# Performance work log

Measured on AMD Instinct MI355X. Metric: run time of the kernel, lower is better.

## Reference

```python
import jax, jax.numpy as jnp
import numpy as np

NUM_CLASSES = 1000
FEAT = 192
HID = 256
TOTAL_NODES = 8192  # 16 images * 512 patches, kNN is global (no batch vector in source)


def _knn_idx(x, k):
    # squared euclidean distances, top-k smallest (self-loop included: d(i,i)=0)
    sq = jnp.sum(x * x, axis=-1)                       # [N]
    d = sq[:, None] + sq[None, :] - 2.0 * (x @ x.T)    # [N, N]
    _, idx = jax.lax.top_k(-d, k)                      # [N, k] neighbor indices per node
    return idx


def _sage_conv(x, idx, w_l, b_l, w_r):
    # PyG SAGEConv (mean aggr): lin_l(mean_j x_j) + lin_r(x_i); bias on lin_l
    agg = jnp.mean(x[idx], axis=1)                     # [N, C_in] mean over k neighbors
    return agg @ w_l + b_l + x @ w_r


def setup_inputs() -> dict:
    key = jax.random.key(0)
    ks = jax.random.split(key, 8)
    s = lambda fi, fo: (2.0 / (fi + fo)) ** 0.5
    return {
        "x": jax.random.normal(ks[0], (TOTAL_NODES, FEAT), dtype=jnp.float32),
        "w_l0": jax.random.normal(ks[1], (FEAT, HID), jnp.float32) * s(FEAT, HID),
        "b_l0": jnp.zeros((HID,), jnp.float32),
        "w_r0": jax.random.normal(ks[2], (FEAT, HID), jnp.float32) * s(FEAT, HID),
        "w_l1": jax.random.normal(ks[3], (HID, HID), jnp.float32) * s(HID, HID),
        "b_l1": jnp.zeros((HID,), jnp.float32),
        "w_r1": jax.random.normal(ks[4], (HID, HID), jnp.float32) * s(HID, HID),
        "w_l2": jax.random.normal(ks[5], (HID, NUM_CLASSES), jnp.float32) * s(HID, NUM_CLASSES),
        "b_l2": jnp.zeros((NUM_CLASSES,), jnp.float32),
        "w_r2": jax.random.normal(ks[6], (HID, NUM_CLASSES), jnp.float32) * s(HID, NUM_CLASSES),
        "k": 9,
        "batch_size": 16,
    }


def reference(x, w_l0, b_l0, w_r0, w_l1, b_l1, w_r1, w_l2, b_l2, w_r2, k, batch_size):
    idx = _knn_idx(x, k)  # graph built once from input features, reused by all layers
    h = jax.nn.relu(_sage_conv(x, idx, w_l0, b_l0, w_r0))
    h = jax.nn.relu(_sage_conv(h, idx, w_l1, b_l1, w_r1))
    h = jax.nn.relu(_sage_conv(h, idx, w_l2, b_l2, w_r2))
    # global_mean_pool with batch = arange(B).repeat_interleave(N/B): equal-size segments
    h = h.reshape(batch_size, -1, h.shape[-1]).mean(axis=1)  # [B, num_classes]
    return h
```

## Files before the change

kernel.cpp:

```cpp
#include <hip/hip_runtime.h>

#define NN   8192
#define FEAT 192
#define HID  256
#define NCLS 1000
#define KNN  9
#define NPP  512
#define NIMG 16
#define KD   192
#define KL0  384

typedef unsigned short ushort_t;
typedef unsigned int uint_t;
typedef __attribute__((ext_vector_type(8))) __bf16 bf16x8;
typedef __attribute__((ext_vector_type(4))) float f32x4;

#define ASYNC16(gptr, lptr)                                                  \
  __builtin_amdgcn_global_load_lds(                                          \
      (const __attribute__((address_space(1))) void*)(gptr),                 \
      (__attribute__((address_space(3))) void*)(lptr), 16, 0, 0)

#define MFMA(a, b, c) __builtin_amdgcn_mfma_f32_16x16x32_bf16((a), (b), (c), 0, 0, 0)

__device__ __forceinline__ ushort_t f2bf_rne(float f) {
  unsigned u = __float_as_uint(f);
  u += 0x7FFF + ((u >> 16) & 1);
  return (ushort_t)(u >> 16);
}
__device__ __forceinline__ float bf2f(ushort_t u) {
  return __uint_as_float((unsigned)u << 16);
}

__device__ __forceinline__ uint_t packkey(float f, int col) {
  uint_t b = __float_as_uint(f);
  uint_t m = (uint_t)((int)b >> 31) | 0x80000000u;
  uint_t u = b ^ m;
  return (u & 0xFFFFE000u) | (uint_t)col;
}

__device__ __forceinline__ uint_t umed3(uint_t a, uint_t b, uint_t c) {
  uint_t d;
  asm("v_med3_u32 %0, %1, %2, %3" : "=v"(d) : "v"(a), "v"(b), "v"(c));
  return d;
}

__device__ __forceinline__ void bubble9(uint_t (&tk)[KNN], uint_t k) {
#pragma unroll
  for (int p = KNN - 1; p > 0; --p) tk[p] = umed3(tk[p - 1], tk[p], k);
  tk[0] = min(tk[0], k);
}

__global__ __launch_bounds__(256) void k_prep(
    const float* __restrict__ x, float* __restrict__ sq,
    ushort_t* __restrict__ xs,
    const float* __restrict__ w_l0, const float* __restrict__ w_r0,
    const float* __restrict__ w_l1, const float* __restrict__ w_r1,
    const float* __restrict__ w_l2, const float* __restrict__ w_r2,
    ushort_t* __restrict__ WT0, ushort_t* __restrict__ WT1,
    ushort_t* __restrict__ WT2, float* __restrict__ out) {
  const int blk = blockIdx.x, t = threadIdx.x;
  if (blk < 2048) {
    int wid  = (blk * 256 + t) >> 6;
    int lane = t & 63;
    const float* row = x + (size_t)wid * FEAT;
    ushort_t* xr = xs + (size_t)wid * KD;
    float s = 0.f;
#pragma unroll
    for (int f0 = 0; f0 < FEAT; f0 += 64) {
      int f = f0 + lane;
      float v = row[f];
      s += v * v;
      xr[f] = f2bf_rne(v);
    }
#pragma unroll
    for (int off = 32; off > 0; off >>= 1) s += __shfl_down(s, off);
    if (lane == 0) sq[wid] = s;
    return;
  }
  int i = (blk - 2048) * 256 + t;
  if (i < NIMG * NCLS) out[i] = 0.f;
  if (i < 98304) {
    int n = i / 384, k = i - n * 384;
    float v = (k < 192) ? w_l0[k * 256 + n] : w_r0[(k - 192) * 256 + n];
    WT0[i] = f2bf_rne(v);
  } else if (i < 98304 + 131072) {
    int j = i - 98304;
    int n = j / 512, k = j - n * 512;
    float v = (k < 256) ? w_l1[k * 256 + n] : w_r1[(k - 256) * 256 + n];
    WT1[j] = f2bf_rne(v);
  } else {
    int j = i - (98304 + 131072);
    int n = j / 512, k = j - n * 512;
    float v = 0.f;
    if (n < NCLS)
      v = (k < 256) ? w_l2[k * NCLS + n] : w_r2[(k - 256) * NCLS + n];
    WT2[j] = f2bf_rne(v);
  }
}

__global__ __launch_bounds__(256, 4) void k_dist_topk(
    const ushort_t* __restrict__ xs, const float* __restrict__ sq,
    uint_t* __restrict__ cand) {
  __shared__ __align__(16) char smem[24576];
  ushort_t* As = (ushort_t*)smem;
  ushort_t* Bs = (ushort_t*)(smem + 8192);
  uint_t*   Ms = (uint_t*)(smem + 19456);

  const int t    = threadIdx.x;
  const int lane = t & 63;
  const int w    = t >> 6;
  const int l15  = lane & 15, lq = lane >> 4;
  const int rowStart = blockIdx.y * 128;
  const int colStart = blockIdx.x * 128;
  const int mrow = (w >> 1) * 64;
  const int ncol = (w & 1) * 64;

  const int m0 = w * 128 + lane;
  const int r0 = m0 >> 2, r1 = r0 + 16;
  const int g0 = m0 & 3;
  const int gs0 = g0 ^ (r0 & 3);
  const int gs1 = g0 ^ (r1 & 3);
  const ushort_t* gA0 = xs + (size_t)(rowStart + r0) * KD + gs0 * 8;
  const ushort_t* gA1 = xs + (size_t)(rowStart + r1) * KD + gs1 * 8;
  const ushort_t* gB0 = xs + (size_t)(colStart + r0) * KD + gs0 * 8;
  const ushort_t* gB1 = xs + (size_t)(colStart + r1) * KD + gs1 * 8;
  ushort_t* lA = As + w * 1024;
  ushort_t* lB = Bs + w * 1024;

  const int pg = (lq ^ (l15 & 3)) * 8;
  int aoff[4], boff[4];
#pragma unroll
  for (int ti = 0; ti < 4; ++ti) aoff[ti] = (mrow + ti * 16 + l15) * 32 + pg;
#pragma unroll
  for (int tj = 0; tj < 4; ++tj) boff[tj] = (ncol + tj * 16 + l15) * 32 + pg;

  f32x4 c00 = {}, c01 = {}, c02 = {}, c03 = {};
  f32x4 c10 = {}, c11 = {}, c12 = {}, c13 = {};
  f32x4 c20 = {}, c21 = {}, c22 = {}, c23 = {};
  f32x4 c30 = {}, c31 = {}, c32 = {}, c33 = {};

#pragma unroll 1
  for (int kt = 0; kt < 6; ++kt) {
    const int k0 = kt * 32;
    ASYNC16(gA0 + k0, lA);
    ASYNC16(gA1 + k0, lA + 512);
    ASYNC16(gB0 + k0, lB);
    ASYNC16(gB1 + k0, lB + 512);
    __syncthreads();
    bf16x8 a0 = *(const bf16x8*)(As + aoff[0]);
    bf16x8 a1 = *(const bf16x8*)(As + aoff[1]);
    bf16x8 a2 = *(const bf16x8*)(As + aoff[2]);
    bf16x8 a3 = *(const bf16x8*)(As + aoff[3]);
    bf16x8 b0 = *(const bf16x8*)(Bs + boff[0]);
    bf16x8 b1 = *(const bf16x8*)(Bs + boff[1]);
    bf16x8 b2 = *(const bf16x8*)(Bs + boff[2]);
    bf16x8 b3 = *(const bf16x8*)(Bs + boff[3]);
    c00 = MFMA(a0, b0, c00); c01 = MFMA(a0, b1, c01);
    c02 = MFMA(a0, b2, c02); c03 = MFMA(a0, b3, c03);
    c10 = MFMA(a1, b0, c10); c11 = MFMA(a1, b1, c11);
    c12 = MFMA(a1, b2, c12); c13 = MFMA(a1, b3, c13);
    c20 = MFMA(a2, b0, c20); c21 = MFMA(a2, b1, c21);
    c22 = MFMA(a2, b2, c22); c23 = MFMA(a2, b3, c23);
    c30 = MFMA(a3, b0, c30); c31 = MFMA(a3, b1, c31);
    c32 = MFMA(a3, b2, c32); c33 = MFMA(a3, b3, c33);
    __syncthreads();
  }

  uint_t tk[KNN];
#pragma unroll
  for (int n = 0; n < KNN; ++n) tk[n] = 0xFFFFFFFFu;

  uint_t* Ew = (uint_t*)smem + w * (64 * 19);

#define EPI_ROW(TI, CV)                                                      \
  do {                                                                       \
    f32x4 v_ = (CV);                                                         \
    Ew[((TI) * 16 + lq * 4 + 0) * 19 + l15] =                                \
        packkey(fmaf(-2.0f, v_.x, sqv), mycol);                              \
    Ew[((TI) * 16 + lq * 4 + 1) * 19 + l15] =                                \
        packkey(fmaf(-2.0f, v_.y, sqv), mycol);                              \
    Ew[((TI) * 16 + lq * 4 + 2) * 19 + l15] =                                \
        packkey(fmaf(-2.0f, v_.z, sqv), mycol);                              \
    Ew[((TI) * 16 + lq * 4 + 3) * 19 + l15] =                                \
        packkey(fmaf(-2.0f, v_.w, sqv), mycol);                              \
  } while (0)

#define EPI_TILE(TJ, C0, C1, C2, C3)                                         \
  do {                                                                       \
    int mycol = colStart + ncol + (TJ) * 16 + l15;                           \
    float sqv = sq[mycol];                                                   \
    EPI_ROW(0, C0); EPI_ROW(1, C1); EPI_ROW(2, C2); EPI_ROW(3, C3);          \
    _Pragma("unroll")                                                        \
    for (int c = 0; c < 16; ++c) bubble9(tk, Ew[lane * 19 + c]);             \
  } while (0)

  EPI_TILE(0, c00, c10, c20, c30);
  EPI_TILE(1, c01, c11, c21, c31);
  EPI_TILE(2, c02, c12, c22, c32);
  EPI_TILE(3, c03, c13, c23, c33);

  __syncthreads();
  if (w & 1) {
#pragma unroll
    for (int n = 0; n < KNN; ++n) Ms[(mrow + lane) * 10 + n] = tk[n];
  }
  __syncthreads();
  if (!(w & 1)) {
#pragma unroll
    for (int n = 0; n < KNN; ++n) bubble9(tk, Ms[(mrow + lane) * 10 + n]);
    size_t base = (((size_t)(rowStart + mrow + lane)) * 64 + blockIdx.x) * KNN;
#pragma unroll
    for (int n = 0; n < KNN; ++n) cand[base + n] = tk[n];
  }
}

__global__ __launch_bounds__(256) void k_reduce_gather(
    const uint_t* __restrict__ cand, const float* __restrict__ x,
    int* __restrict__ idx, ushort_t* __restrict__ Ab0) {
  int wid  = (blockIdx.x * 256 + threadIdx.x) >> 6;
  int lane = threadIdx.x & 63;
  if (wid >= NN) return;
  const uint_t* cv = cand + (size_t)wid * 576;
  uint_t tk[KNN];
#pragma unroll
  for (int n = 0; n < KNN; ++n) tk[n] = 0xFFFFFFFFu;
#pragma unroll
  for (int m = 0; m < KNN; ++m) bubble9(tk, cv[lane + 64 * m]);

  int nb[KNN];
  for (int r = 0; r < KNN; ++r) {
    uint_t bm = tk[0];
#pragma unroll
    for (int off = 32; off > 0; off >>= 1)
      bm = min(bm, (uint_t)__shfl_xor((unsigned int)bm, off));
    if (tk[0] == bm) {
#pragma unroll
      for (int p = 0; p < KNN - 1; ++p) tk[p] = tk[p + 1];
      tk[KNN - 1] = 0xFFFFFFFFu;
    }
    nb[r] = (int)(bm & 0x1FFFu);
    if (lane == 0) idx[wid * KNN + r] = nb[r];
  }

#pragma unroll
  for (int f0 = 0; f0 < FEAT; f0 += 64) {
    int f = f0 + lane;
    float s = 0.f;
#pragma unroll
    for (int n = 0; n < KNN; ++n) s += x[(size_t)nb[n] * FEAT + f];
    Ab0[(size_t)wid * KL0 + f]        = f2bf_rne(s * (1.0f / KNN));
    Ab0[(size_t)wid * KL0 + FEAT + f] = f2bf_rne(x[(size_t)wid * FEAT + f]);
  }
}

__global__ __launch_bounds__(256) void k_gather_h(
    const ushort_t* __restrict__ hsrc, const int* __restrict__ idx,
    ushort_t* __restrict__ adst) {
  const int t = threadIdx.x;
  const int lane = t & 63, w = t >> 6;
  const int r  = (blockIdx.x * 4 + w) * 2 + (lane >> 5);
  const int cl = (lane & 31) * 8;
  int nb[KNN];
#pragma unroll
  for (int n = 0; n < KNN; ++n) nb[n] = idx[r * KNN + n];
  float s[8] = {};
#pragma unroll
  for (int n = 0; n < KNN; ++n) {
    uint4 v = *(const uint4*)(hsrc + (size_t)nb[n] * 512 + cl);
    s[0] += __uint_as_float(v.x << 16); s[1] += __uint_as_float(v.x & 0xFFFF0000u);
    s[2] += __uint_as_float(v.y << 16); s[3] += __uint_as_float(v.y & 0xFFFF0000u);
    s[4] += __uint_as_float(v.z << 16); s[5] += __uint_as_float(v.z & 0xFFFF0000u);
    s[6] += __uint_as_float(v.w << 16); s[7] += __uint_as_float(v.w & 0xFFFF0000u);
  }
  uint4 o;
  o.x = (uint_t)f2bf_rne(s[0] * (1.0f / KNN)) |
        ((uint_t)f2bf_rne(s[1] * (1.0f / KNN)) << 16);
  o.y = (uint_t)f2bf_rne(s[2] * (1.0f / KNN)) |
        ((uint_t)f2bf_rne(s[3] * (1.0f / KNN)) << 16);
  o.z = (uint_t)f2bf_rne(s[4] * (1.0f / KNN)) |
        ((uint_t)f2bf_rne(s[5] * (1.0f / KNN)) << 16);
  o.w = (uint_t)f2bf_rne(s[6] * (1.0f / KNN)) |
        ((uint_t)f2bf_rne(s[7] * (1.0f / KNN)) << 16);
  *(uint4*)(adst + (size_t)r * 512 + cl) = o;
}

__global__ __launch_bounds__(256) void k_sage64(
    const ushort_t* __restrict__ Ab, const ushort_t* __restrict__ WT,
    const float* __restrict__ bias, ushort_t* __restrict__ hdst, int KT) {
  __shared__ __align__(16) char smem[8192];
  ushort_t* As = (ushort_t*)smem;
  ushort_t* Bs = (ushort_t*)(smem + 4096);
  const int blk = blockIdx.x;
  const int t = threadIdx.x;
  const int lane = t & 63, w = t >> 6;
  const int l15 = lane & 15, lq = lane >> 4;
  const int rowStart = (blk >> 2) * 64, colStart = (blk & 3) * 64;
  const int mrow = (w >> 1) * 32, ncol = (w & 1) * 32;

  const int rA = t >> 2, g = t & 3;
  const int gs = g ^ (rA & 3);
  const ushort_t* gA = Ab + (size_t)(rowStart + rA) * KT + gs * 8;
  const ushort_t* gB = WT + (size_t)(colStart + rA) * KT + gs * 8;
  ushort_t* lA = As + w * 512;
  ushort_t* lB = Bs + w * 512;

  const int pg = (lq ^ (l15 & 3)) * 8;
  const int aoff0 = (mrow + l15) * 32 + pg, aoff1 = (mrow + 16 + l15) * 32 + pg;
  const int boff0 = (ncol + l15) * 32 + pg, boff1 = (ncol + 16 + l15) * 32 + pg;

  f32x4 c00 = {}, c01 = {}, c10 = {}, c11 = {};
  const int nkt = KT >> 5;
#pragma unroll 1
  for (int kt = 0; kt < nkt; ++kt) {
    const int k0 = kt * 32;
    ASYNC16(gA + k0, lA);
    ASYNC16(gB + k0, lB);
    __syncthreads();
    bf16x8 a0 = *(const bf16x8*)(As + aoff0);
    bf16x8 a1 = *(const bf16x8*)(As + aoff1);
    bf16x8 b0 = *(const bf16x8*)(Bs + boff0);
    bf16x8 b1 = *(const bf16x8*)(Bs + boff1);
    c00 = MFMA(a0, b0, c00); c01 = MFMA(a0, b1, c01);
    c10 = MFMA(a1, b0, c10); c11 = MFMA(a1, b1, c11);
    __syncthreads();
  }

  const float bv0 = bias[colStart + ncol + l15];
  const float bv1 = bias[colStart + ncol + 16 + l15];
#define S64_ST(TI, TJ, CV, BV)                                               \
  do {                                                                       \
    f32x4 v_ = (CV);                                                         \
    int col_ = colStart + ncol + (TJ) * 16 + l15;                            \
    size_t rb_ = (size_t)(rowStart + mrow + (TI) * 16 + lq * 4);             \
    hdst[(rb_ + 0) * 512 + col_] = f2bf_rne(fmaxf(v_.x + (BV), 0.f));        \
    hdst[(rb_ + 1) * 512 + col_] = f2bf_rne(fmaxf(v_.y + (BV), 0.f));        \
    hdst[(rb_ + 2) * 512 + col_] = f2bf_rne(fmaxf(v_.z + (BV), 0.f));        \
    hdst[(rb_ + 3) * 512 + col_] = f2bf_rne(fmaxf(v_.w + (BV), 0.f));        \
  } while (0)
  S64_ST(0, 0, c00, bv0); S64_ST(0, 1, c01, bv1);
  S64_ST(1, 0, c10, bv0); S64_ST(1, 1, c11, bv1);
}

__global__ __launch_bounds__(256, 2) void k_sage128_pool(
    const ushort_t* __restrict__ Ab, const ushort_t* __restrict__ WT,
    const float* __restrict__ bias, float* __restrict__ out) {
  __shared__ __align__(16) char smem[16384];
  ushort_t* As = (ushort_t*)smem;
  ushort_t* Bs = (ushort_t*)(smem + 8192);
  __shared__ float Ps[2][128];

  const int t    = threadIdx.x;
  const int lane = t & 63;
  const int w    = t >> 6;
  const int l15  = lane & 15, lq = lane >> 4;
  const int rowStart = blockIdx.y * 128;
  const int colStart = blockIdx.x * 128;
  const int mrow = (w >> 1) * 64;
  const int ncol = (w & 1) * 64;
  const int KT = 512;

  const int rA0 = t >> 2, rA1 = rA0 + 64;
  const int g = t & 3;
  const int gsA0 = g ^ (rA0 & 3), gsA1 = g ^ (rA1 & 3);
  const ushort_t* gA0 = Ab + (size_t)(rowStart + rA0) * KT + gsA0 * 8;
  const ushort_t* gA1 = Ab + (size_t)(rowStart + rA1) * KT + gsA1 * 8;
  const ushort_t* gB0 = WT + (size_t)(colStart + rA0) * KT + gsA0 * 8;
  const ushort_t* gB1 = WT + (size_t)(colStart + rA1) * KT + gsA1 * 8;
  ushort_t* lA0 = As + w * 512;
  ushort_t* lA1 = As + 2048 + w * 512;
  ushort_t* lB0 = Bs + w * 512;
  ushort_t* lB1 = Bs + 2048 + w * 512;

  const int pg = (lq ^ (l15 & 3)) * 8;
  int aoff[4], boff[4];
#pragma unroll
  for (int ti = 0; ti < 4; ++ti) aoff[ti] = (mrow + ti * 16 + l15) * 32 + pg;
#pragma unroll
  for (int tj = 0; tj < 4; ++tj) boff[tj] = (ncol + tj * 16 + l15) * 32 + pg;

  f32x4 c00 = {}, c01 = {}, c02 = {}, c03 = {};
  f32x4 c10 = {}, c11 = {}, c12 = {}, c13 = {};
  f32x4 c20 = {}, c21 = {}, c22 = {}, c23 = {};
  f32x4 c30 = {}, c31 = {}, c32 = {}, c33 = {};

#pragma unroll 1
  for (int kt = 0; kt < 16; ++kt) {
    const int k0 = kt * 32;
    ASYNC16(gA0 + k0, lA0);
    ASYNC16(gA1 + k0, lA1);
    ASYNC16(gB0 + k0, lB0);
    ASYNC16(gB1 + k0, lB1);
    __syncthreads();
    bf16x8 a0 = *(const bf16x8*)(As + aoff[0]);
    bf16x8 a1 = *(const bf16x8*)(As + aoff[1]);
    bf16x8 a2 = *(const bf16x8*)(As + aoff[2]);
    bf16x8 a3 = *(const bf16x8*)(As + aoff[3]);
    bf16x8 b0v = *(const bf16x8*)(Bs + boff[0]);
    bf16x8 b1v = *(const bf16x8*)(Bs + boff[1]);
    bf16x8 b2v = *(const bf16x8*)(Bs + boff[2]);
    bf16x8 b3v = *(const bf16x8*)(Bs + boff[3]);
    c00 = MFMA(a0, b0v, c00); c01 = MFMA(a0, b1v, c01);
    c02 = MFMA(a0, b2v, c02); c03 = MFMA(a0, b3v, c03);
    c10 = MFMA(a1, b0v, c10); c11 = MFMA(a1, b1v, c11);
    c12 = MFMA(a1, b2v, c12); c13 = MFMA(a1, b3v, c13);
    c20 = MFMA(a2, b0v, c20); c21 = MFMA(a2, b1v, c21);
    c22 = MFMA(a2, b2v, c22); c23 = MFMA(a2, b3v, c23);
    c30 = MFMA(a3, b0v, c30); c31 = MFMA(a3, b1v, c31);
    c32 = MFMA(a3, b2v, c32); c33 = MFMA(a3, b3v, c33);
    __syncthreads();
  }

#define P_ACC(CV)                                                            \
  (fmaxf((CV).x + bv_, 0.f) + fmaxf((CV).y + bv_, 0.f) +                     \
   fmaxf((CV).z + bv_, 0.f) + fmaxf((CV).w + bv_, 0.f))

#define POOL_COL(TJ, C0, C1, C2, C3)                                         \
  do {                                                                       \
    int col_ = colStart + ncol + (TJ) * 16 + l15;                            \
    float bv_ = (col_ < NCLS) ? bias[col_] : 0.f;                            \
    float s_ = P_ACC(C0) + P_ACC(C1) + P_ACC(C2) + P_ACC(C3);                \
    s_ += __shfl_xor(s_, 16);                                                \
    s_ += __shfl_xor(s_, 32);                                                \
    if (lq == 0) Ps[w >> 1][ncol + (TJ) * 16 + l15] = s_;                    \
  } while (0)

  POOL_COL(0, c00, c10, c20, c30);
  POOL_COL(1, c01, c11, c21, c31);
  POOL_COL(2, c02, c12, c22, c32);
  POOL_COL(3, c03, c13, c23, c33);

  __syncthreads();
  if (t < 128) {
    int col = colStart + t;
    if (col < NCLS) {
      float s = Ps[0][t] + Ps[1][t];
      int img = rowStart / NPP;
      atomicAdd(out + (size_t)img * NCLS + col, s * (1.0f / NPP));
    }
  }
}

extern "C" void kernel_launch(void* const* d_in, const int* in_sizes, int n_in,
                              void* d_out, int out_size, void* d_ws,
                              size_t ws_size, hipStream_t stream) {
  const float* x    = (const float*)d_in[0];
  const float* w_l0 = (const float*)d_in[1];
  const float* b_l0 = (const float*)d_in[2];
  const float* w_r0 = (const float*)d_in[3];
  const float* w_l1 = (const float*)d_in[4];
  const float* b_l1 = (const float*)d_in[5];
  const float* w_r1 = (const float*)d_in[6];
  const float* w_l2 = (const float*)d_in[7];
  const float* b_l2 = (const float*)d_in[8];
  const float* w_r2 = (const float*)d_in[9];
  float* out = (float*)d_out;

  char* ws = (char*)d_ws;
  float*    sq   = (float*)(ws);
  int*      idx  = (int*)(ws + 32768);
  uint_t*   cand = (uint_t*)(ws + 327680);
  ushort_t* xs   = (ushort_t*)(ws + 19202048);
  ushort_t* Ab0  = (ushort_t*)(ws + 22347776);
  ushort_t* WT0  = (ushort_t*)(ws + 28639232);
  ushort_t* WT1  = (ushort_t*)(ws + 28835840);
  ushort_t* WT2  = (ushort_t*)(ws + 29097984);
  ushort_t* Ab1  = (ushort_t*)(ws + 327680);
  ushort_t* Ab2  = (ushort_t*)(ws + 8716288);

  k_prep<<<4992, 256, 0, stream>>>(x, sq, xs, w_l0, w_r0, w_l1, w_r1,
                                   w_l2, w_r2, WT0, WT1, WT2, out);
  k_dist_topk<<<dim3(64, 64), 256, 0, stream>>>(xs, sq, cand);
  k_reduce_gather<<<2048, 256, 0, stream>>>(cand, x, idx, Ab0);
  k_sage64<<<512, 256, 0, stream>>>(Ab0, WT0, b_l0, Ab1 + 256, KL0);
  k_gather_h<<<1024, 256, 0, stream>>>(Ab1 + 256, idx, Ab1);
  k_sage64<<<512, 256, 0, stream>>>(Ab1, WT1, b_l1, Ab2 + 256, 512);
  k_gather_h<<<1024, 256, 0, stream>>>(Ab2 + 256, idx, Ab2);
  k_sage128_pool<<<dim3(8, 64), 256, 0, stream>>>(Ab2, WT2, b_l2, out);
}
```

Baseline: 183.1 us.

## Process two column tiles per distance block and double K-step in SAGE GEMMs

```diff
diff --git a/kernel.cpp b/kernel.cpp
--- a/kernel.cpp
+++ b/kernel.cpp
@@ -9,6 +9,7 @@
 #define NIMG 16
 #define KD   192
 #define KL0  384
+#define NCB  32
 
 typedef unsigned short ushort_t;
 typedef unsigned int uint_t;
@@ -111,7 +112,7 @@
   const int w    = t >> 6;
   const int l15  = lane & 15, lq = lane >> 4;
   const int rowStart = blockIdx.y * 128;
-  const int colStart = blockIdx.x * 128;
+  const int colBase  = blockIdx.x * 256;
   const int mrow = (w >> 1) * 64;
   const int ncol = (w & 1) * 64;
 
@@ -122,8 +123,6 @@
   const int gs1 = g0 ^ (r1 & 3);
   const ushort_t* gA0 = xs + (size_t)(rowStart + r0) * KD + gs0 * 8;
   const ushort_t* gA1 = xs + (size_t)(rowStart + r1) * KD + gs1 * 8;
-  const ushort_t* gB0 = xs + (size_t)(colStart + r0) * KD + gs0 * 8;
-  const ushort_t* gB1 = xs + (size_t)(colStart + r1) * KD + gs1 * 8;
   ushort_t* lA = As + w * 1024;
   ushort_t* lB = Bs + w * 1024;
 
@@ -134,43 +133,49 @@
 #pragma unroll
   for (int tj = 0; tj < 4; ++tj) boff[tj] = (ncol + tj * 16 + l15) * 32 + pg;
 
-  f32x4 c00 = {}, c01 = {}, c02 = {}, c03 = {};
-  f32x4 c10 = {}, c11 = {}, c12 = {}, c13 = {};
-  f32x4 c20 = {}, c21 = {}, c22 = {}, c23 = {};
-  f32x4 c30 = {}, c31 = {}, c32 = {}, c33 = {};
+  uint_t tk[KNN];
+#pragma unroll
+  for (int n = 0; n < KNN; ++n) tk[n] = 0xFFFFFFFFu;
+
+  uint_t* Ew = (uint_t*)smem + w * (64 * 19);
 
 #pragma unroll 1
-  for (int kt = 0; kt < 6; ++kt) {
-    const int k0 = kt * 32;
-    ASYNC16(gA0 + k0, lA);
-    ASYNC16(gA1 + k0, lA + 512);
-    ASYNC16(gB0 + k0, lB);
-    ASYNC16(gB1 + k0, lB + 512);
-    __syncthreads();
-    bf16x8 a0 = *(const bf16x8*)(As + aoff[0]);
-    bf16x8 a1 = *(const bf16x8*)(As + aoff[1]);
-    bf16x8 a2 = *(const bf16x8*)(As + aoff[2]);
-    bf16x8 a3 = *(const bf16x8*)(As + aoff[3]);
-    bf16x8 b0 = *(const bf16x8*)(Bs + boff[0]);
-    bf16x8 b1 = *(const bf16x8*)(Bs + boff[1]);
-    bf16x8 b2 = *(const bf16x8*)(Bs + boff[2]);
-    bf16x8 b3 = *(const bf16x8*)(Bs + boff[3]);
-    c00 = MFMA(a0, b0, c00); c01 = MFMA(a0, b1, c01);
-    c02 = MFMA(a0, b2, c02); c03 = MFMA(a0, b3, c03);
-    c10 = MFMA(a1, b0, c10); c11 = MFMA(a1, b1, c11);
-    c12 = MFMA(a1, b2, c12); c13 = MFMA(a1, b3, c13);
-    c20 = MFMA(a2, b0, c20); c21 = MFMA(a2, b1, c21);
-    c22 = MFMA(a2, b2, c22); c23 = MFMA(a2, b3, c23);
-    c30 = MFMA(a3, b0, c30); c31 = MFMA(a3, b1, c31);
-    c32 = MFMA(a3, b2, c32); c33 = MFMA(a3, b3, c33);
-    __syncthreads();
-  }
-
-  uint_t tk[KNN];
-#pragma unroll
-  for (int n = 0; n < KNN; ++n) tk[n] = 0xFFFFFFFFu;
-
-  uint_t* Ew = (uint_t*)smem + w * (64 * 19);
+  for (int ct = 0; ct < 2; ++ct) {
+    const int colStart = colBase + ct * 128;
+    const ushort_t* gB0 = xs + (size_t)(colStart + r0) * KD + gs0 * 8;
+    const ushort_t* gB1 = xs + (size_t)(colStart + r1) * KD + gs1 * 8;
+
+    f32x4 c00 = {}, c01 = {}, c02 = {}, c03 = {};
+    f32x4 c10 = {}, c11 = {}, c12 = {}, c13 = {};
+    f32x4 c20 = {}, c21 = {}, c22 = {}, c23 = {};
+    f32x4 c30 = {}, c31 = {}, c32 = {}, c33 = {};
+
+#pragma unroll 1
+    for (int kt = 0; kt < 6; ++kt) {
+      const int k0 = kt * 32;
+      ASYNC16(gA0 + k0, lA);
+      ASYNC16(gA1 + k0, lA + 512);
+      ASYNC16(gB0 + k0, lB);
+      ASYNC16(gB1 + k0, lB + 512);
+      __syncthreads();
+      bf16x8 a0 = *(const bf16x8*)(As + aoff[0]);
+      bf16x8 a1 = *(const bf16x8*)(As + aoff[1]);
+      bf16x8 a2 = *(const bf16x8*)(As + aoff[2]);
+      bf16x8 a3 = *(const bf16x8*)(As + aoff[3]);
+      bf16x8 b0 = *(const bf16x8*)(Bs + boff[0]);
+      bf16x8 b1 = *(const bf16x8*)(Bs + boff[1]);
+      bf16x8 b2 = *(const bf16x8*)(Bs + boff[2]);
+      bf16x8 b3 = *(const bf16x8*)(Bs + boff[3]);
+      c00 = MFMA(a0, b0, c00); c01 = MFMA(a0, b1, c01);
+      c02 = MFMA(a0, b2, c02); c03 = MFMA(a0, b3, c03);
+      c10 = MFMA(a1, b0, c10); c11 = MFMA(a1, b1, c11);
+      c12 = MFMA(a1, b2, c12); c13 = MFMA(a1, b3, c13);
+      c20 = MFMA(a2, b0, c20); c21 = MFMA(a2, b1, c21);
+      c22 = MFMA(a2, b2, c22); c23 = MFMA(a2, b3, c23);
+      c30 = MFMA(a3, b0, c30); c31 = MFMA(a3, b1, c31);
+      c32 = MFMA(a3, b2, c32); c33 = MFMA(a3, b3, c33);
+      __syncthreads();
+    }
 
 #define EPI_ROW(TI, CV)                                                      \
   do {                                                                       \
@@ -194,12 +199,14 @@
     for (int c = 0; c < 16; ++c) bubble9(tk, Ew[lane * 19 + c]);             \
   } while (0)
 
-  EPI_TILE(0, c00, c10, c20, c30);
-  EPI_TILE(1, c01, c11, c21, c31);
-  EPI_TILE(2, c02, c12, c22, c32);
-  EPI_TILE(3, c03, c13, c23, c33);
-
-  __syncthreads();
+    EPI_TILE(0, c00, c10, c20, c30);
+    EPI_TILE(1, c01, c11, c21, c31);
+    EPI_TILE(2, c02, c12, c22, c32);
+    EPI_TILE(3, c03, c13, c23, c33);
+
+    __syncthreads();
+  }
+
   if (w & 1) {
 #pragma unroll
     for (int n = 0; n < KNN; ++n) Ms[(mrow + lane) * 10 + n] = tk[n];
@@ -208,7 +215,8 @@
   if (!(w & 1)) {
 #pragma unroll
     for (int n = 0; n < KNN; ++n) bubble9(tk, Ms[(mrow + lane) * 10 + n]);
-    size_t base = (((size_t)(rowStart + mrow + lane)) * 64 + blockIdx.x) * KNN;
+    size_t base =
+        (((size_t)(rowStart + mrow + lane)) * NCB + blockIdx.x) * KNN;
 #pragma unroll
     for (int n = 0; n < KNN; ++n) cand[base + n] = tk[n];
   }
@@ -220,12 +228,13 @@
   int wid  = (blockIdx.x * 256 + threadIdx.x) >> 6;
   int lane = threadIdx.x & 63;
   if (wid >= NN) return;
-  const uint_t* cv = cand + (size_t)wid * 576;
+  const uint_t* cv = cand + (size_t)wid * (NCB * KNN);
   uint_t tk[KNN];
 #pragma unroll
   for (int n = 0; n < KNN; ++n) tk[n] = 0xFFFFFFFFu;
 #pragma unroll
-  for (int m = 0; m < KNN; ++m) bubble9(tk, cv[lane + 64 * m]);
+  for (int m = 0; m < 4; ++m) bubble9(tk, cv[lane + 64 * m]);
+  bubble9(tk, (lane < 32) ? cv[lane + 256] : 0xFFFFFFFFu);
 
   int nb[KNN];
   for (int r = 0; r < KNN; ++r) {
@@ -287,9 +296,9 @@
 __global__ __launch_bounds__(256) void k_sage64(
     const ushort_t* __restrict__ Ab, const ushort_t* __restrict__ WT,
     const float* __restrict__ bias, ushort_t* __restrict__ hdst, int KT) {
-  __shared__ __align__(16) char smem[8192];
+  __shared__ __align__(16) char smem[16384];
   ushort_t* As = (ushort_t*)smem;
-  ushort_t* Bs = (ushort_t*)(smem + 4096);
+  ushort_t* Bs = (ushort_t*)(smem + 8192);
   const int blk = blockIdx.x;
   const int t = threadIdx.x;
   const int lane = t & 63, w = t >> 6;
@@ -309,12 +318,14 @@
   const int boff0 = (ncol + l15) * 32 + pg, boff1 = (ncol + 16 + l15) * 32 + pg;
 
   f32x4 c00 = {}, c01 = {}, c10 = {}, c11 = {};
-  const int nkt = KT >> 5;
+  const int nkt = KT >> 6;
 #pragma unroll 1
   for (int kt = 0; kt < nkt; ++kt) {
-    const int k0 = kt * 32;
+    const int k0 = kt * 64;
     ASYNC16(gA + k0, lA);
+    ASYNC16(gA + k0 + 32, lA + 2048);
     ASYNC16(gB + k0, lB);
+    ASYNC16(gB + k0 + 32, lB + 2048);
     __syncthreads();
     bf16x8 a0 = *(const bf16x8*)(As + aoff0);
     bf16x8 a1 = *(const bf16x8*)(As + aoff1);
@@ -322,6 +333,12 @@
     bf16x8 b1 = *(const bf16x8*)(Bs + boff1);
     c00 = MFMA(a0, b0, c00); c01 = MFMA(a0, b1, c01);
     c10 = MFMA(a1, b0, c10); c11 = MFMA(a1, b1, c11);
+    bf16x8 a0p = *(const bf16x8*)(As + 2048 + aoff0);
+    bf16x8 a1p = *(const bf16x8*)(As + 2048 + aoff1);
+    bf16x8 b0p = *(const bf16x8*)(Bs + 2048 + boff0);
+    bf16x8 b1p = *(const bf16x8*)(Bs + 2048 + boff1);
+    c00 = MFMA(a0p, b0p, c00); c01 = MFMA(a0p, b1p, c01);
+    c10 = MFMA(a1p, b0p, c10); c11 = MFMA(a1p, b1p, c11);
     __syncthreads();
   }
 
@@ -344,9 +361,9 @@
 __global__ __launch_bounds__(256, 2) void k_sage128_pool(
     const ushort_t* __restrict__ Ab, const ushort_t* __restrict__ WT,
     const float* __restrict__ bias, float* __restrict__ out) {
-  __shared__ __align__(16) char smem[16384];
+  __shared__ __align__(16) char smem[32768];
   ushort_t* As = (ushort_t*)smem;
-  ushort_t* Bs = (ushort_t*)(smem + 8192);
+  ushort_t* Bs = (ushort_t*)(smem + 16384);
   __shared__ float Ps[2][128];
 
   const int t    = threadIdx.x;
@@ -383,30 +400,40 @@
   f32x4 c20 = {}, c21 = {}, c22 = {}, c23 = {};
   f32x4 c30 = {}, c31 = {}, c32 = {}, c33 = {};
 
+#define POOL_MFMA_PANEL(OFS)                                                 \
+  do {                                                                       \
+    bf16x8 a0 = *(const bf16x8*)(As + (OFS) + aoff[0]);                      \
+    bf16x8 a1 = *(const bf16x8*)(As + (OFS) + aoff[1]);                      \
+    bf16x8 a2 = *(const bf16x8*)(As + (OFS) + aoff[2]);                      \
+    bf16x8 a3 = *(const bf16x8*)(As + (OFS) + aoff[3]);                      \
+    bf16x8 b0v = *(const bf16x8*)(Bs + (OFS) + boff[0]);                     \
+    bf16x8 b1v = *(const bf16x8*)(Bs + (OFS) + boff[1]);                     \
+    bf16x8 b2v = *(const bf16x8*)(Bs + (OFS) + boff[2]);                     \
+    bf16x8 b3v = *(const bf16x8*)(Bs + (OFS) + boff[3]);                     \
+    c00 = MFMA(a0, b0v, c00); c01 = MFMA(a0, b1v, c01);                      \
+    c02 = MFMA(a0, b2v, c02); c03 = MFMA(a0, b3v, c03);                      \
+    c10 = MFMA(a1, b0v, c10); c11 = MFMA(a1, b1v, c11);                      \
+    c12 = MFMA(a1, b2v, c12); c13 = MFMA(a1, b3v, c13);                      \
+    c20 = MFMA(a2, b0v, c20); c21 = MFMA(a2, b1v, c21);                      \
+    c22 = MFMA(a2, b2v, c22); c23 = MFMA(a2, b3v, c23);                      \
+    c30 = MFMA(a3, b0v, c30); c31 = MFMA(a3, b1v, c31);                      \
+    c32 = MFMA(a3, b2v, c32); c33 = MFMA(a3, b3v, c33);                      \
+  } while (0)
+
 #pragma unroll 1
-  for (int kt = 0; kt < 16; ++kt) {
-    const int k0 = kt * 32;
+  for (int kt = 0; kt < 8; ++kt) {
+    const int k0 = kt * 64;
     ASYNC16(gA0 + k0, lA0);
     ASYNC16(gA1 + k0, lA1);
+    ASYNC16(gA0 + k0 + 32, lA0 + 4096);
+    ASYNC16(gA1 + k0 + 32, lA1 + 4096);
     ASYNC16(gB0 + k0, lB0);
     ASYNC16(gB1 + k0, lB1);
+    ASYNC16(gB0 + k0 + 32, lB0 + 4096);
+    ASYNC16(gB1 + k0 + 32, lB1 + 4096);
     __syncthreads();
-    bf16x8 a0 = *(const bf16x8*)(As + aoff[0]);
-    bf16x8 a1 = *(const bf16x8*)(As + aoff[1]);
-    bf16x8 a2 = *(const bf16x8*)(As + aoff[2]);
-    bf16x8 a3 = *(const bf16x8*)(As + aoff[3]);
-    bf16x8 b0v = *(const bf16x8*)(Bs + boff[0]);
-    bf16x8 b1v = *(const bf16x8*)(Bs + boff[1]);
-    bf16x8 b2v = *(const bf16x8*)(Bs + boff[2]);
-    bf16x8 b3v = *(const bf16x8*)(Bs + boff[3]);
-    c00 = MFMA(a0, b0v, c00); c01 = MFMA(a0, b1v, c01);
-    c02 = MFMA(a0, b2v, c02); c03 = MFMA(a0, b3v, c03);
-    c10 = MFMA(a1, b0v, c10); c11 = MFMA(a1, b1v, c11);
-    c12 = MFMA(a1, b2v, c12); c13 = MFMA(a1, b3v, c13);
-    c20 = MFMA(a2, b0v, c20); c21 = MFMA(a2, b1v, c21);
-    c22 = MFMA(a2, b2v, c22); c23 = MFMA(a2, b3v, c23);
-    c30 = MFMA(a3, b0v, c30); c31 = MFMA(a3, b1v, c31);
-    c32 = MFMA(a3, b2v, c32); c33 = MFMA(a3, b3v, c33);
+    POOL_MFMA_PANEL(0);
+    POOL_MFMA_PANEL(4096);
     __syncthreads();
   }
 
@@ -469,7 +496,7 @@
 
   k_prep<<<4992, 256, 0, stream>>>(x, sq, xs, w_l0, w_r0, w_l1, w_r1,
                                    w_l2, w_r2, WT0, WT1, WT2, out);
-  k_dist_topk<<<dim3(64, 64), 256, 0, stream>>>(xs, sq, cand);
+  k_dist_topk<<<dim3(NCB, 64), 256, 0, stream>>>(xs, sq, cand);
   k_reduce_gather<<<2048, 256, 0, stream>>>(cand, x, idx, Ab0);
   k_sage64<<<512, 256, 0, stream>>>(Ab0, WT0, b_l0, Ab1 + 256, KL0);
   k_gather_h<<<1024, 256, 0, stream>>>(Ab1 + 256, idx, Ab1);
```

New measurement: 183.6 us. Within noise of the previous version (+0.2%).
